# Kernel optimization log

Hardware: AMD Instinct MI355X
Metric: run time of the kernel (lower is better)

Reference implementation:

```python
import jax, jax.numpy as jnp
import numpy as np

H = 128
TYPES = ['user', 'news', 'source', 'follower']
N = {'user': 200000, 'news': 100000, 'source': 5000, 'follower': 200000}
IN = {'user': 128, 'news': 300, 'source': 128, 'follower': 128}
OUT = 2
# relation r: REL_SRC[r] -> REL_DST[r]; order: posts, posted_by, publishes, published_by, follows, followed_by
REL_SRC = ['user', 'news', 'source', 'news', 'follower', 'user']
REL_DST = ['news', 'user', 'news', 'source', 'user', 'follower']
DST_RELS = {'user': [1, 4], 'news': [0, 2], 'source': [3], 'follower': [5]}
E_POSTS, E_PUB, E_FOL = 500000, 100000, 1000000


def _graph_conv(h_src, src, dst, n_src, n_dst, W, b):
    # DGL GraphConv, norm='both': D_dst^{-1/2} A D_src^{-1/2} X W + b (degrees clamped at 1)
    ones = jnp.ones(src.shape[0], h_src.dtype)
    deg_out = jnp.maximum(jax.ops.segment_sum(ones, src, num_segments=n_src), 1.0)
    deg_in = jnp.maximum(jax.ops.segment_sum(ones, dst, num_segments=n_dst), 1.0)
    msg = (h_src * jax.lax.rsqrt(deg_out)[:, None])[src]  # [E, H] gather
    agg = jax.ops.segment_sum(msg, dst, num_segments=n_dst) * jax.lax.rsqrt(deg_in)[:, None]
    return agg @ W + b


def _hetero(ktype, h, edges, Wset, bset):
    # HeteroGraphConv aggregate='mean': mean over relations whose dst type is ktype
    outs = [_graph_conv(h[REL_SRC[r]], edges[r][0], edges[r][1], N[REL_SRC[r]], N[ktype], Wset[r], bset[r])
            for r in DST_RELS[ktype]]
    return sum(outs) / len(outs)


def setup_inputs():
    key = jax.random.key(0)
    ks = iter(jax.random.split(key, 40))
    d = {}
    for t in TYPES:
        d['x_' + t] = jax.random.normal(next(ks), (N[t], IN[t]), jnp.float32)
    for t in TYPES:
        d['Wi1_' + t] = jax.random.normal(next(ks), (IN[t], H), jnp.float32) / np.sqrt(IN[t]).astype(np.float32)
        d['bi1_' + t] = jnp.zeros((H,), jnp.float32)
    d['Wi2'] = jax.random.normal(next(ks), (4, H, H), jnp.float32) / np.float32(np.sqrt(H))
    d['bi2'] = jnp.zeros((4, H), jnp.float32)
    for name in ['conv1', 'conv2']:
        d[name + '_W'] = jax.random.normal(next(ks), (4, 6, H, H), jnp.float32) / np.float32(np.sqrt(H))
        d[name + '_b'] = jnp.zeros((4, 6, H), jnp.float32)
    for t in TYPES:
        d['Wl_' + t] = jax.random.normal(next(ks), (H, OUT), jnp.float32) / np.float32(np.sqrt(H))
        d['bl_' + t] = jnp.zeros((OUT,), jnp.float32)
    d['posts_u'] = jax.random.randint(next(ks), (E_POSTS,), 0, N['user'])
    d['posts_n'] = jax.random.randint(next(ks), (E_POSTS,), 0, N['news'])
    d['pub_s'] = jax.random.randint(next(ks), (E_PUB,), 0, N['source'])
    d['pub_n'] = jax.random.randint(next(ks), (E_PUB,), 0, N['news'])
    d['fol_f'] = jax.random.randint(next(ks), (E_FOL,), 0, N['follower'])
    d['fol_u'] = jax.random.randint(next(ks), (E_FOL,), 0, N['user'])
    return d


def reference(x_user, x_news, x_source, x_follower,
              Wi1_user, bi1_user, Wi1_news, bi1_news, Wi1_source, bi1_source, Wi1_follower, bi1_follower,
              Wi2, bi2, conv1_W, conv1_b, conv2_W, conv2_b,
              Wl_user, bl_user, Wl_news, bl_news, Wl_source, bl_source, Wl_follower, bl_follower,
              posts_u, posts_n, pub_s, pub_n, fol_f, fol_u):
    lrelu = lambda v: jax.nn.leaky_relu(v, 0.01)
    edges = [(posts_u, posts_n), (posts_n, posts_u), (pub_s, pub_n),
             (pub_n, pub_s), (fol_f, fol_u), (fol_u, fol_f)]
    x = {'user': x_user, 'news': x_news, 'source': x_source, 'follower': x_follower}
    Wi1 = {'user': Wi1_user, 'news': Wi1_news, 'source': Wi1_source, 'follower': Wi1_follower}
    bi1 = {'user': bi1_user, 'news': bi1_news, 'source': bi1_source, 'follower': bi1_follower}
    Wl = {'user': Wl_user, 'news': Wl_news, 'source': Wl_source, 'follower': Wl_follower}
    bl = {'user': bl_user, 'news': bl_news, 'source': bl_source, 'follower': bl_follower}
    h = {t: lrelu(x[t] @ Wi1[t] + bi1[t]) for t in TYPES}
    h = {t: lrelu(h[t] @ Wi2[i] + bi2[i]) for i, t in enumerate(TYPES)}
    h = {t: lrelu(_hetero(t, h, edges, conv1_W[i], conv1_b[i])) for i, t in enumerate(TYPES)}
    h1 = {t: lrelu(_hetero(t, h, edges, conv2_W[i], conv2_b[i])) for i, t in enumerate(TYPES)}
    out = {t: h1[t] @ Wl[t] + bl[t] for t in TYPES}
    # original returns ({type: logits}, {type: h1}); flatten to a tuple in TYPES order
    return tuple(out[t] for t in TYPES) + tuple(h1[t] for t in TYPES)
```

## Files before the change

### kernel.cpp

```cpp
#include <hip/hip_runtime.h>

typedef unsigned short u16;
typedef unsigned int   u32;
using short8  = __attribute__((ext_vector_type(8))) short;
using short4v = __attribute__((ext_vector_type(4))) short;
using f32x4   = __attribute__((ext_vector_type(4))) float;
using f32x2   = __attribute__((ext_vector_type(2))) float;

#define N_USER 200000
#define N_NEWS 100000
#define N_SRCT 5000
#define N_FOLW 200000
#define E_POSTS 500000
#define E_PUB   100000
#define E_FOLL  1000000
#define NCNT    805000
#define NPOOL   3200000

__device__ __forceinline__ float bf2f(u16 h) {
  union { u32 u; float f; } v; v.u = ((u32)h) << 16; return v.f;
}
__device__ __forceinline__ u16 f2bf(float f) {
  union { float f; u32 u; } v; v.f = f;
  u32 r = v.u + 0x7FFFu + ((v.u >> 16) & 1u);
  return (u16)(r >> 16);
}

__global__ void count_k(const int* __restrict__ idx, int n, int* __restrict__ cnt) {
  int i = blockIdx.x * 256 + threadIdx.x;
  if (i < n) atomicAdd(&cnt[idx[i]], 1);
}
__global__ void rsqrt_k(const int* __restrict__ cnti, float* __restrict__ out, int n) {
  int i = blockIdx.x * 256 + threadIdx.x;
  if (i < n) {
    int c = cnti[i];
    out[i] = rsqrtf((float)(c > 0 ? c : 1));
  }
}

__global__ void scan1_k(const int* __restrict__ in, int* __restrict__ out,
                        int* __restrict__ bsum, int n) {
  __shared__ int s[256];
  int tid = threadIdx.x;
  int gid = blockIdx.x * 256 + tid;
  int v = (gid < n) ? in[gid] : 0;
  s[tid] = v;
  __syncthreads();
  for (int d = 1; d < 256; d <<= 1) {
    int t = (tid >= d) ? s[tid - d] : 0;
    __syncthreads();
    s[tid] += t;
    __syncthreads();
  }
  if (gid < n) out[gid] = s[tid];
  if (tid == 255) bsum[blockIdx.x] = s[255];
}
__global__ void scan2_k(int* __restrict__ bsum, int m) {
  __shared__ int p[256];
  __shared__ int buf[3328];
  int tid = threadIdx.x;
  int chunk = (m + 255) / 256;
  int run = 0;
  for (int i = 0; i < chunk; ++i) {
    int idx = tid * chunk + i;
    int v = (idx < m) ? bsum[idx] : 0;
    if (idx < m) buf[idx] = run;
    run += v;
  }
  p[tid] = run;
  __syncthreads();
  int own = run;
  for (int d = 1; d < 256; d <<= 1) {
    int t = (tid >= d) ? p[tid - d] : 0;
    __syncthreads();
    p[tid] += t;
    __syncthreads();
  }
  int base = p[tid] - own;
  for (int i = 0; i < chunk; ++i) {
    int idx = tid * chunk + i;
    if (idx < m) bsum[idx] = buf[idx] + base;
  }
}
__global__ void scan3_k(int* __restrict__ offs, const int* __restrict__ cnti,
                        const int* __restrict__ bsum, int n) {
  int gid = blockIdx.x * 256 + threadIdx.x;
  if (gid < n) offs[gid] = offs[gid] - cnti[gid] + bsum[blockIdx.x];
}

__global__ void csr_fill_k(const int* __restrict__ src, const int* __restrict__ dst,
                           const int* __restrict__ offs, int* __restrict__ curs,
                           int* __restrict__ pool, int E, int cntOff) {
  int e = blockIdx.x * 256 + threadIdx.x;
  if (e >= E) return;
  int d = dst[e] + cntOff;
  int p = offs[d] + atomicAdd(&curs[d], 1);
  pool[p] = src[e];
}

__global__ void cvt_pad8_k(const float* __restrict__ X, u16* __restrict__ P,
                           int Ksrc, int Kdst, int total8) {
  int i = blockIdx.x * 256 + threadIdx.x;
  if (i >= total8) return;
  int base = i * 8;
  short8 o;
  if (Ksrc == Kdst) {
    f32x4 a = *(const f32x4*)(X + base);
    f32x4 b = *(const f32x4*)(X + base + 4);
#pragma unroll
    for (int j = 0; j < 4; ++j) { o[j] = (short)f2bf(a[j]); o[j + 4] = (short)f2bf(b[j]); }
  } else {
    int row = base / Kdst;
    int k = base - row * Kdst;
#pragma unroll
    for (int j = 0; j < 8; ++j) {
      int kk = k + j;
      o[j] = (kk < Ksrc) ? (short)f2bf(X[(size_t)row * Ksrc + kk]) : (short)0;
    }
  }
  *(short8*)(P + base) = o;
}

__global__ void trans_w_k(const float* __restrict__ W, u16* __restrict__ WT,
                          int Ksrc, int Kdst, int total) {
  int i = blockIdx.x * 256 + threadIdx.x;
  if (i >= total) return;
  int per = Kdst << 7;
  int m = i / per, rem = i - m * per;
  int n = rem / Kdst, k = rem - n * Kdst;
  WT[i] = (k < Ksrc) ? f2bf(W[(size_t)m * Ksrc * 128 + (size_t)k * 128 + n]) : (u16)0;
}

__global__ __launch_bounds__(256, 2) void gemm_bf16(
    const u16* __restrict__ A, int lda, int M, int K,
    const u16* __restrict__ WT,
    const float* __restrict__ bias,
    const float* __restrict__ rowscale,
    u16* __restrict__ C, int leaky)
{
  __shared__ u16 Ws[128][136];
  const int tid  = threadIdx.x;
  const int wave = tid >> 6;
  const int lane = tid & 63;
  const int l15  = lane & 15;
  const int l4   = lane >> 4;
  const int rowBase = blockIdx.x * 128 + wave * 32;

  f32x4 acc[2][8];
#pragma unroll
  for (int g = 0; g < 2; ++g)
#pragma unroll
    for (int c = 0; c < 8; ++c) acc[g][c] = (f32x4){0.f, 0.f, 0.f, 0.f};

  const int r0 = (rowBase + l15 < M) ? rowBase + l15 : M - 1;
  const int r1 = (rowBase + 16 + l15 < M) ? rowBase + 16 + l15 : M - 1;

  for (int kb = 0; kb < K; kb += 128) {
    const int chunkK = (K - kb < 128) ? (K - kb) : 128;
    __syncthreads();
    for (int fl = tid * 8; fl < (chunkK << 7); fl += 2048) {
      int n = fl / chunkK;
      int kk = fl - n * chunkK;
      *(short8*)(&Ws[n][kk]) = *(const short8*)(WT + (size_t)n * K + kb + kk);
    }
    __syncthreads();
    const int nsteps = chunkK >> 5;
    for (int ks = 0; ks < nsteps; ++ks) {
      const int kg = ks * 32 + l4 * 8;
      short8 a0 = *(const short8*)(A + (size_t)r0 * lda + kb + kg);
      short8 a1 = *(const short8*)(A + (size_t)r1 * lda + kb + kg);
#pragma unroll
      for (int c = 0; c < 8; ++c) {
        short8 b = *(const short8*)(&Ws[c * 16 + l15][kg]);
        acc[0][c] = __builtin_amdgcn_mfma_f32_16x16x32_bf16(a0, b, acc[0][c], 0, 0, 0);
        acc[1][c] = __builtin_amdgcn_mfma_f32_16x16x32_bf16(a1, b, acc[1][c], 0, 0, 0);
      }
    }
  }

  float bvals[8];
#pragma unroll
  for (int c = 0; c < 8; ++c) bvals[c] = bias ? bias[c * 16 + l15] : 0.f;

#pragma unroll
  for (int g = 0; g < 2; ++g) {
#pragma unroll
    for (int r = 0; r < 4; ++r) {
      int row = rowBase + g * 16 + l4 * 4 + r;
      if (row >= M) continue;
      float sc = rowscale ? rowscale[row] : 1.f;
#pragma unroll
      for (int c = 0; c < 8; ++c) {
        float v = acc[g][c][r] * sc + bvals[c];
        if (leaky) v = (v > 0.f) ? v : 0.01f * v;
        C[(size_t)row * 128 + c * 16 + l15] = f2bf(v);
      }
    }
  }
}

__global__ __launch_bounds__(256) void gather_conv(
    const u16* __restrict__ T, const int* __restrict__ pool,
    const int* __restrict__ offs, const int* __restrict__ cnti,
    const float* __restrict__ rsin,
    int co0, int to0, int co1, int to1,
    const float* __restrict__ b1, const float* __restrict__ b2, float invn,
    u16* __restrict__ out_bf, float* __restrict__ out_f, int nDst)
{
  const int wave = threadIdx.x >> 6;
  const int lane = threadIdx.x & 63;
  const int sub  = lane >> 4;
  const int l15  = lane & 15;
  const int d = blockIdx.x * 4 + wave;
  if (d >= nDst) return;

  float s[8];
#pragma unroll
  for (int j = 0; j < 8; ++j) s[j] = 0.f;

  int co = co0, to = to0;
#pragma unroll 1
  for (int r = 0; r < 2; ++r) {
    if (co < 0) break;
    const int off = offs[co + d];
    const int cnt = cnti[co + d];
    const float sc = rsin[co + d];
    float p[8];
#pragma unroll
    for (int j = 0; j < 8; ++j) p[j] = 0.f;
#pragma unroll 1
    for (int e = 0; e < cnt; e += 4) {
      int ee = e + sub;
      bool valid = ee < cnt;
      int idx = pool[off + (valid ? ee : cnt - 1)];
      short8 w = *(const short8*)(T + (((size_t)(to + idx)) << 7) + l15 * 8);
      if (valid) {
#pragma unroll
        for (int j = 0; j < 8; ++j) p[j] += bf2f((u16)w[j]);
      }
    }
#pragma unroll
    for (int j = 0; j < 8; ++j) s[j] += p[j] * sc;
    co = co1; to = to1;
  }

#pragma unroll
  for (int j = 0; j < 8; ++j) {
    s[j] += __shfl_xor(s[j], 16, 64);
    s[j] += __shfl_xor(s[j], 32, 64);
  }

  if (sub == 0) {
    const int col = l15 * 8;
    float v[8];
#pragma unroll
    for (int j = 0; j < 8; ++j) {
      float bb = b1[col + j] + (b2 ? b2[col + j] : 0.f);
      float x = (s[j] + bb) * invn;
      v[j] = (x > 0.f) ? x : 0.01f * x;
    }
    if (out_f) {
      float* op = out_f + (((size_t)d) << 7) + col;
      *(f32x4*)op       = (f32x4){v[0], v[1], v[2], v[3]};
      *(f32x4*)(op + 4) = (f32x4){v[4], v[5], v[6], v[7]};
    } else {
      short8 o;
#pragma unroll
      for (int j = 0; j < 8; ++j) o[j] = (short)f2bf(v[j]);
      *(short8*)(out_bf + (((size_t)d) << 7) + col) = o;
    }
  }
}

__global__ __launch_bounds__(256) void linear_k(
    const float* __restrict__ H, const float* __restrict__ Wl,
    const float* __restrict__ bl, float* __restrict__ OUT, int rows)
{
  __shared__ float w0[128], w1[128];
  int tid = threadIdx.x;
  if (tid < 128) { w0[tid] = Wl[tid * 2]; w1[tid] = Wl[tid * 2 + 1]; }
  __syncthreads();
  int row = blockIdx.x * 256 + tid;
  if (row >= rows) return;
  const float* hp = H + ((size_t)row << 7);
  float s0 = 0.f, s1 = 0.f;
#pragma unroll
  for (int k = 0; k < 128; k += 4) {
    f32x4 h4 = *(const f32x4*)(hp + k);
#pragma unroll
    for (int j = 0; j < 4; ++j) {
      s0 += h4[j] * w0[k + j];
      s1 += h4[j] * w1[k + j];
    }
  }
  OUT[(size_t)row * 2]     = s0 + bl[0];
  OUT[(size_t)row * 2 + 1] = s1 + bl[1];
}

extern "C" void kernel_launch(void* const* d_in, const int* in_sizes, int n_in,
                              void* d_out, int out_size, void* d_ws, size_t ws_size,
                              hipStream_t stream)
{
  (void)in_sizes; (void)n_in; (void)out_size; (void)ws_size;

  char* wp = (char*)d_ws;
  auto take = [&](size_t bytes) { void* p = wp; wp += (bytes + 255) & ~(size_t)255; return p; };
  u16*   ARENA = (u16*)take(206080000);
  u16*   HA  = (u16*)take(129280000);
  u16*   HB  = (u16*)take(129280000);
  u16*   WTA = (u16*)take(1884160);
  float* CNT = (float*)take(3220000);
  int*   CNTI = (int*)take(3220000);
  int*   OFFS = (int*)take(3220000);
  int*   CURS = (int*)take(3220000);
  int*   POOL = (int*)take(12800000);
  int*   BSUM = (int*)take(16384);
  u16*   XB  = ARENA;
  u16*   TP  = ARENA;

  const int rowOff[4] = {0, 200000, 300000, 305000};
  const int Nt[4]     = {N_USER, N_NEWS, N_SRCT, N_FOLW};
  const size_t XOFF[4] = {0, 25600000, 57600000, 58240000};
  const int KD[4] = {128, 320, 128, 128};
  const int KS[4] = {128, 300, 128, 128};
  const int WT1[4] = {0, 16384, 57344, 73728};
  const int WT2 = 90112, WTC1 = 155648, WTC2 = 548864;

  struct RelG { int E, srcIdx, dstIdx, srcType, dstType, srcCnt, dstCnt, tOff; };
  const RelG rels[6] = {
    {E_POSTS, 26, 27, 0, 1, 0,      200000, 0},
    {E_POSTS, 27, 26, 1, 0, 200000, 0,      200000},
    {E_PUB,   28, 29, 2, 1, 300000, 305000, 300000},
    {E_PUB,   29, 28, 1, 2, 305000, 300000, 305000},
    {E_FOLL,  30, 31, 3, 0, 405000, 605000, 405000},
    {E_FOLL,  31, 30, 0, 3, 605000, 405000, 605000},
  };

  hipMemsetAsync(CNTI, 0, NCNT * 4, stream);
  count_k<<<(E_POSTS + 255) / 256, 256, 0, stream>>>((const int*)d_in[26], E_POSTS, CNTI + 0);
  count_k<<<(E_POSTS + 255) / 256, 256, 0, stream>>>((const int*)d_in[27], E_POSTS, CNTI + 200000);
  count_k<<<(E_PUB   + 255) / 256, 256, 0, stream>>>((const int*)d_in[28], E_PUB,   CNTI + 300000);
  count_k<<<(E_PUB   + 255) / 256, 256, 0, stream>>>((const int*)d_in[29], E_PUB,   CNTI + 305000);
  count_k<<<(E_FOLL  + 255) / 256, 256, 0, stream>>>((const int*)d_in[30], E_FOLL,  CNTI + 405000);
  count_k<<<(E_FOLL  + 255) / 256, 256, 0, stream>>>((const int*)d_in[31], E_FOLL,  CNTI + 605000);
  rsqrt_k<<<(NCNT + 255) / 256, 256, 0, stream>>>(CNTI, CNT, NCNT);

  const int scanBlocks = (NCNT + 255) / 256;
  scan1_k<<<scanBlocks, 256, 0, stream>>>(CNTI, OFFS, BSUM, NCNT);
  scan2_k<<<1, 256, 0, stream>>>(BSUM, scanBlocks);
  scan3_k<<<scanBlocks, 256, 0, stream>>>(OFFS, CNTI, BSUM, NCNT);
  hipMemsetAsync(CURS, 0, NCNT * 4, stream);
  for (int r = 0; r < 6; ++r) {
    csr_fill_k<<<(rels[r].E + 255) / 256, 256, 0, stream>>>(
        (const int*)d_in[rels[r].srcIdx], (const int*)d_in[rels[r].dstIdx],
        OFFS, CURS, POOL, rels[r].E, rels[r].dstCnt);
  }

  for (int t = 0; t < 4; ++t) {
    int total8 = (Nt[t] * KD[t]) / 8;
    cvt_pad8_k<<<(total8 + 255) / 256, 256, 0, stream>>>(
        (const float*)d_in[t], XB + XOFF[t], KS[t], KD[t], total8);
  }
  auto transL = [&](int idx, int wtOff, int Ksrc, int Kdst, int total) {
    trans_w_k<<<(total + 255) / 256, 256, 0, stream>>>(
        (const float*)d_in[idx], WTA + wtOff, Ksrc, Kdst, total);
  };
  transL(4,  WT1[0], 128, 128, 16384);
  transL(6,  WT1[1], 300, 320, 40960);
  transL(8,  WT1[2], 128, 128, 16384);
  transL(10, WT1[3], 128, 128, 16384);
  transL(12, WT2,    128, 128, 65536);
  transL(14, WTC1,   128, 128, 393216);
  transL(16, WTC2,   128, 128, 393216);

  auto gemmL = [&](const u16* A, int lda, int M, int K, const u16* WTp,
                   const float* bias, const float* rs, u16* C, int leaky) {
    gemm_bf16<<<(M + 127) / 128, 256, 0, stream>>>(A, lda, M, K, WTp, bias, rs, C, leaky);
  };

  for (int t = 0; t < 4; ++t)
    gemmL(XB + XOFF[t], KD[t], Nt[t], KD[t], WTA + WT1[t],
          (const float*)d_in[5 + 2 * t], nullptr, HA + (size_t)rowOff[t] * 128, 1);

  for (int t = 0; t < 4; ++t)
    gemmL(HA + (size_t)rowOff[t] * 128, 128, Nt[t], 128, WTA + WT2 + t * 16384,
          (const float*)d_in[13] + t * 128, nullptr, HB + (size_t)rowOff[t] * 128, 1);

  const size_t H1OFF[4] = {1010000, 26610000, 39410000, 40050000};
  const size_t LOFF[4]  = {0, 400000, 600000, 610000};
  const int relsOf[4][2] = {{1, 4}, {0, 2}, {3, -1}, {5, -1}};
  float* OUT = (float*)d_out;

  for (int layer = 0; layer < 2; ++layer) {
    const u16* HIn     = layer ? HA : HB;
    const u16* wt      = WTA + (layer ? WTC2 : WTC1);
    const float* convb = (const float*)d_in[layer ? 17 : 15];
    for (int r = 0; r < 6; ++r) {
      const RelG& q = rels[r];
      gemmL(HIn + (size_t)rowOff[q.srcType] * 128, 128, Nt[q.srcType], 128,
            wt + (size_t)(q.dstType * 6 + r) * 16384, nullptr, CNT + q.srcCnt,
            TP + (size_t)q.tOff * 128, 0);
    }
    for (int k = 0; k < 4; ++k) {
      int r1 = relsOf[k][0], r2 = relsOf[k][1];
      int co0 = rels[r1].dstCnt, to0 = rels[r1].tOff;
      int co1 = (r2 >= 0) ? rels[r2].dstCnt : -1;
      int to1 = (r2 >= 0) ? rels[r2].tOff : 0;
      const float* b1 = convb + (size_t)(k * 6 + r1) * 128;
      const float* b2 = (r2 >= 0) ? convb + (size_t)(k * 6 + r2) * 128 : nullptr;
      float invn = (r2 >= 0) ? 0.5f : 1.0f;
      u16* obf  = layer ? nullptr : (HA + (size_t)rowOff[k] * 128);
      float* of = layer ? (OUT + H1OFF[k]) : nullptr;
      gather_conv<<<(Nt[k] + 3) / 4, 256, 0, stream>>>(
          TP, POOL, OFFS, CNTI, CNT, co0, to0, co1, to1, b1, b2, invn, obf, of, Nt[k]);
    }
  }

  for (int k = 0; k < 4; ++k)
    linear_k<<<(Nt[k] + 255) / 256, 256, 0, stream>>>(
        OUT + H1OFF[k], (const float*)d_in[18 + 2 * k], (const float*)d_in[19 + 2 * k],
        OUT + LOFF[k], Nt[k]);
}
```

Measured before the change: 2.280 ms.

## Batch preprocessing launches, fuse fp32 input conversion into GEMM, merge gather loops

Several per-relation and per-type launches (degree counting, CSR fill, weight transposes, final linear heads) are folded into single multi-segment kernels to cut launch overhead. The first-layer GEMM now reads fp32 inputs directly and converts them to bf16 in registers, which removes the separate conversion pass and its intermediate buffer. The gather kernel walks both relations in one flat loop with two edges per lane group per iteration, aiming for more memory parallelism. Relation GEMMs are reordered to run just before their consumer gather, which may improve cache locality. In exchange, the GEMM A-loads become fp32 with conversion work, and the boundary constants are hardcoded.

```diff
diff --git a/kernel.cpp b/kernel.cpp
--- a/kernel.cpp
+++ b/kernel.cpp
@@ -26,9 +26,19 @@
   return (u16)(r >> 16);
 }
 
-__global__ void count_k(const int* __restrict__ idx, int n, int* __restrict__ cnt) {
+__global__ void count6_k(const int* __restrict__ p0, const int* __restrict__ p1,
+                         const int* __restrict__ p2, const int* __restrict__ p3,
+                         const int* __restrict__ p4, const int* __restrict__ p5,
+                         int* __restrict__ cnt) {
   int i = blockIdx.x * 256 + threadIdx.x;
-  if (i < n) atomicAdd(&cnt[idx[i]], 1);
+  const int* p; int off;
+  if      (i < 500000)  { p = p0; off = 0; }
+  else if (i < 1000000) { p = p1; i -= 500000;  off = 200000; }
+  else if (i < 1100000) { p = p2; i -= 1000000; off = 300000; }
+  else if (i < 1200000) { p = p3; i -= 1100000; off = 305000; }
+  else if (i < 2200000) { p = p4; i -= 1200000; off = 405000; }
+  else                  { p = p5; i -= 2200000; off = 605000; }
+  atomicAdd(&cnt[off + p[i]], 1);
 }
 __global__ void rsqrt_k(const int* __restrict__ cnti, float* __restrict__ out, int n) {
   int i = blockIdx.x * 256 + threadIdx.x;
@@ -88,51 +98,71 @@
   if (gid < n) offs[gid] = offs[gid] - cnti[gid] + bsum[blockIdx.x];
 }
 
-__global__ void csr_fill_k(const int* __restrict__ src, const int* __restrict__ dst,
-                           const int* __restrict__ offs, int* __restrict__ curs,
-                           int* __restrict__ pool, int E, int cntOff) {
-  int e = blockIdx.x * 256 + threadIdx.x;
-  if (e >= E) return;
-  int d = dst[e] + cntOff;
-  int p = offs[d] + atomicAdd(&curs[d], 1);
-  pool[p] = src[e];
-}
-
-__global__ void cvt_pad8_k(const float* __restrict__ X, u16* __restrict__ P,
-                           int Ksrc, int Kdst, int total8) {
+__global__ void fill6_k(const int* __restrict__ s0, const int* __restrict__ d0,
+                        const int* __restrict__ s1, const int* __restrict__ d1,
+                        const int* __restrict__ s2, const int* __restrict__ d2,
+                        const int* __restrict__ s3, const int* __restrict__ d3,
+                        const int* __restrict__ s4, const int* __restrict__ d4,
+                        const int* __restrict__ s5, const int* __restrict__ d5,
+                        const int* __restrict__ offs, int* __restrict__ curs,
+                        int* __restrict__ pool) {
   int i = blockIdx.x * 256 + threadIdx.x;
-  if (i >= total8) return;
-  int base = i * 8;
-  short8 o;
-  if (Ksrc == Kdst) {
-    f32x4 a = *(const f32x4*)(X + base);
-    f32x4 b = *(const f32x4*)(X + base + 4);
-#pragma unroll
-    for (int j = 0; j < 4; ++j) { o[j] = (short)f2bf(a[j]); o[j + 4] = (short)f2bf(b[j]); }
-  } else {
-    int row = base / Kdst;
-    int k = base - row * Kdst;
-#pragma unroll
-    for (int j = 0; j < 8; ++j) {
-      int kk = k + j;
-      o[j] = (kk < Ksrc) ? (short)f2bf(X[(size_t)row * Ksrc + kk]) : (short)0;
-    }
-  }
-  *(short8*)(P + base) = o;
-}
-
+  const int* sp; const int* dp; int off;
+  if      (i < 500000)  { sp = s0; dp = d0; off = 200000; }
+  else if (i < 1000000) { sp = s1; dp = d1; i -= 500000;  off = 0; }
+  else if (i < 1100000) { sp = s2; dp = d2; i -= 1000000; off = 305000; }
+  else if (i < 1200000) { sp = s3; dp = d3; i -= 1100000; off = 300000; }
+  else if (i < 2200000) { sp = s4; dp = d4; i -= 1200000; off = 605000; }
+  else                  { sp = s5; dp = d5; i -= 2200000; off = 405000; }
+  int dd = dp[i] + off;
+  int p = offs[dd] + atomicAdd(&curs[dd], 1);
+  pool[p] = sp[i];
+}
+
+__global__ void trans55_k(const float* __restrict__ w0, const float* __restrict__ w1,
+                          const float* __restrict__ w2, const float* __restrict__ w3,
+                          const float* __restrict__ w4, const float* __restrict__ w5,
+                          u16* __restrict__ WT) {
+  int i = blockIdx.x * 256 + threadIdx.x;
+  int m = i >> 14, rem = i & 16383;
+  int n = rem >> 7, k = rem & 127;
+  const float* W; int lm, dstOff;
+  if      (m < 1)  { W = w0; lm = m;      dstOff = 0; }
+  else if (m < 2)  { W = w1; lm = m - 1;  dstOff = 57344; }
+  else if (m < 3)  { W = w2; lm = m - 2;  dstOff = 73728; }
+  else if (m < 7)  { W = w3; lm = m - 3;  dstOff = 90112; }
+  else if (m < 31) { W = w4; lm = m - 7;  dstOff = 155648; }
+  else             { W = w5; lm = m - 31; dstOff = 548864; }
+  WT[dstOff + (lm << 14) + (n << 7) + k] = f2bf(W[(size_t)(lm << 14) + (k << 7) + n]);
+}
 __global__ void trans_w_k(const float* __restrict__ W, u16* __restrict__ WT,
                           int Ksrc, int Kdst, int total) {
   int i = blockIdx.x * 256 + threadIdx.x;
   if (i >= total) return;
-  int per = Kdst << 7;
-  int m = i / per, rem = i - m * per;
-  int n = rem / Kdst, k = rem - n * Kdst;
-  WT[i] = (k < Ksrc) ? f2bf(W[(size_t)m * Ksrc * 128 + (size_t)k * 128 + n]) : (u16)0;
+  int n = i / Kdst, k = i - n * Kdst;
+  WT[i] = (k < Ksrc) ? f2bf(W[(size_t)k * 128 + n]) : (u16)0;
+}
+
+__device__ __forceinline__ short8 ldA32(const float* __restrict__ rowp, int Ks, int k0) {
+  short8 a;
+  if (k0 + 8 <= Ks) {
+    f32x4 u = *(const f32x4*)(rowp + k0);
+    f32x4 v = *(const f32x4*)(rowp + k0 + 4);
+#pragma unroll
+    for (int j = 0; j < 4; ++j) { a[j] = (short)f2bf(u[j]); a[j + 4] = (short)f2bf(v[j]); }
+  } else {
+#pragma unroll
+    for (int j = 0; j < 8; ++j) {
+      int kk = k0 + j;
+      a[j] = (kk < Ks) ? (short)f2bf(rowp[kk]) : (short)0;
+    }
+  }
+  return a;
 }
 
 __global__ __launch_bounds__(256, 2) void gemm_bf16(
-    const u16* __restrict__ A, int lda, int M, int K,
+    const u16* __restrict__ A, const float* __restrict__ A32, int Ks,
+    int lda, int M, int K,
     const u16* __restrict__ WT,
     const float* __restrict__ bias,
     const float* __restrict__ rowscale,
@@ -167,8 +197,14 @@
     const int nsteps = chunkK >> 5;
     for (int ks = 0; ks < nsteps; ++ks) {
       const int kg = ks * 32 + l4 * 8;
-      short8 a0 = *(const short8*)(A + (size_t)r0 * lda + kb + kg);
-      short8 a1 = *(const short8*)(A + (size_t)r1 * lda + kb + kg);
+      short8 a0, a1;
+      if (A32) {
+        a0 = ldA32(A32 + (size_t)r0 * lda, Ks, kb + kg);
+        a1 = ldA32(A32 + (size_t)r1 * lda, Ks, kb + kg);
+      } else {
+        a0 = *(const short8*)(A + (size_t)r0 * lda + kb + kg);
+        a1 = *(const short8*)(A + (size_t)r1 * lda + kb + kg);
+      }
 #pragma unroll
       for (int c = 0; c < 8; ++c) {
         short8 b = *(const short8*)(&Ws[c * 16 + l15][kg]);
@@ -214,34 +250,40 @@
   const int d = blockIdx.x * 4 + wave;
   if (d >= nDst) return;
 
+  const int off0 = offs[co0 + d];
+  const int cnt0 = cnti[co0 + d];
+  const float sc0 = rsin[co0 + d];
+  int off1 = 0, cnt1 = 0; float sc1 = 0.f;
+  if (co1 >= 0) { off1 = offs[co1 + d]; cnt1 = cnti[co1 + d]; sc1 = rsin[co1 + d]; }
+  const int tot = cnt0 + cnt1;
+
   float s[8];
 #pragma unroll
   for (int j = 0; j < 8; ++j) s[j] = 0.f;
 
-  int co = co0, to = to0;
-#pragma unroll 1
-  for (int r = 0; r < 2; ++r) {
-    if (co < 0) break;
-    const int off = offs[co + d];
-    const int cnt = cnti[co + d];
-    const float sc = rsin[co + d];
-    float p[8];
-#pragma unroll
-    for (int j = 0; j < 8; ++j) p[j] = 0.f;
-#pragma unroll 1
-    for (int e = 0; e < cnt; e += 4) {
-      int ee = e + sub;
-      bool valid = ee < cnt;
-      int idx = pool[off + (valid ? ee : cnt - 1)];
-      short8 w = *(const short8*)(T + (((size_t)(to + idx)) << 7) + l15 * 8);
-      if (valid) {
-#pragma unroll
-        for (int j = 0; j < 8; ++j) p[j] += bf2f((u16)w[j]);
-      }
-    }
-#pragma unroll
-    for (int j = 0; j < 8; ++j) s[j] += p[j] * sc;
-    co = co1; to = to1;
+  for (int e = 0; e < tot; e += 8) {
+    const int eA = e + sub;
+    const int eB = e + 4 + sub;
+    if (eA < tot) {
+      bool f0 = eA < cnt0;
+      int pi = f0 ? (off0 + eA) : (off1 + (eA - cnt0));
+      float sc = f0 ? sc0 : sc1;
+      int tb = f0 ? to0 : to1;
+      int idx = pool[pi];
+      short8 w = *(const short8*)(T + (((size_t)(tb + idx)) << 7) + l15 * 8);
+#pragma unroll
+      for (int j = 0; j < 8; ++j) s[j] += bf2f((u16)w[j]) * sc;
+    }
+    if (eB < tot) {
+      bool f0 = eB < cnt0;
+      int pi = f0 ? (off0 + eB) : (off1 + (eB - cnt0));
+      float sc = f0 ? sc0 : sc1;
+      int tb = f0 ? to0 : to1;
+      int idx = pool[pi];
+      short8 w = *(const short8*)(T + (((size_t)(tb + idx)) << 7) + l15 * 8);
+#pragma unroll
+      for (int j = 0; j < 8; ++j) s[j] += bf2f((u16)w[j]) * sc;
+    }
   }
 
 #pragma unroll
@@ -272,29 +314,47 @@
   }
 }
 
-__global__ __launch_bounds__(256) void linear_k(
-    const float* __restrict__ H, const float* __restrict__ Wl,
-    const float* __restrict__ bl, float* __restrict__ OUT, int rows)
+__global__ __launch_bounds__(256) void linear_all_k(
+    const float* __restrict__ Wu, const float* __restrict__ bu,
+    const float* __restrict__ Wn, const float* __restrict__ bn,
+    const float* __restrict__ Wsrc, const float* __restrict__ bsrc,
+    const float* __restrict__ Wf, const float* __restrict__ bfo,
+    float* __restrict__ OUT)
 {
-  __shared__ float w0[128], w1[128];
+  __shared__ float wsh[4][2][128];
+  __shared__ float bsh[4][2];
   int tid = threadIdx.x;
-  if (tid < 128) { w0[tid] = Wl[tid * 2]; w1[tid] = Wl[tid * 2 + 1]; }
+  if (tid < 128) {
+    wsh[0][0][tid] = Wu[tid * 2];   wsh[0][1][tid] = Wu[tid * 2 + 1];
+    wsh[1][0][tid] = Wn[tid * 2];   wsh[1][1][tid] = Wn[tid * 2 + 1];
+    wsh[2][0][tid] = Wsrc[tid * 2]; wsh[2][1][tid] = Wsrc[tid * 2 + 1];
+    wsh[3][0][tid] = Wf[tid * 2];   wsh[3][1][tid] = Wf[tid * 2 + 1];
+  } else if (tid < 132) {
+    int t = tid - 128;
+    const float* bp = (t == 0) ? bu : (t == 1) ? bn : (t == 2) ? bsrc : bfo;
+    bsh[t][0] = bp[0]; bsh[t][1] = bp[1];
+  }
   __syncthreads();
   int row = blockIdx.x * 256 + tid;
-  if (row >= rows) return;
-  const float* hp = H + ((size_t)row << 7);
+  if (row >= 505000) return;
+  int t, lr; size_t hoff; int loff;
+  if      (row < 200000) { t = 0; lr = row;          hoff = 1010000;  loff = 0; }
+  else if (row < 300000) { t = 1; lr = row - 200000; hoff = 26610000; loff = 400000; }
+  else if (row < 305000) { t = 2; lr = row - 300000; hoff = 39410000; loff = 600000; }
+  else                   { t = 3; lr = row - 305000; hoff = 40050000; loff = 610000; }
+  const float* hp = OUT + hoff + (size_t)lr * 128;
   float s0 = 0.f, s1 = 0.f;
 #pragma unroll
   for (int k = 0; k < 128; k += 4) {
     f32x4 h4 = *(const f32x4*)(hp + k);
 #pragma unroll
     for (int j = 0; j < 4; ++j) {
-      s0 += h4[j] * w0[k + j];
-      s1 += h4[j] * w1[k + j];
-    }
-  }
-  OUT[(size_t)row * 2]     = s0 + bl[0];
-  OUT[(size_t)row * 2 + 1] = s1 + bl[1];
+      s0 += h4[j] * wsh[t][0][k + j];
+      s1 += h4[j] * wsh[t][1][k + j];
+    }
+  }
+  OUT[(size_t)loff + lr * 2]     = s0 + bsh[t][0];
+  OUT[(size_t)loff + lr * 2 + 1] = s1 + bsh[t][1];
 }
 
 extern "C" void kernel_launch(void* const* d_in, const int* in_sizes, int n_in,
@@ -305,7 +365,7 @@
 
   char* wp = (char*)d_ws;
   auto take = [&](size_t bytes) { void* p = wp; wp += (bytes + 255) & ~(size_t)255; return p; };
-  u16*   ARENA = (u16*)take(206080000);
+  u16*   TP  = (u16*)take(206080000);
   u16*   HA  = (u16*)take(129280000);
   u16*   HB  = (u16*)take(129280000);
   u16*   WTA = (u16*)take(1884160);
@@ -315,12 +375,9 @@
   int*   CURS = (int*)take(3220000);
   int*   POOL = (int*)take(12800000);
   int*   BSUM = (int*)take(16384);
-  u16*   XB  = ARENA;
-  u16*   TP  = ARENA;
 
   const int rowOff[4] = {0, 200000, 300000, 305000};
   const int Nt[4]     = {N_USER, N_NEWS, N_SRCT, N_FOLW};
-  const size_t XOFF[4] = {0, 25600000, 57600000, 58240000};
   const int KD[4] = {128, 320, 128, 128};
   const int KS[4] = {128, 300, 128, 128};
   const int WT1[4] = {0, 16384, 57344, 73728};
@@ -337,12 +394,9 @@
   };
 
   hipMemsetAsync(CNTI, 0, NCNT * 4, stream);
-  count_k<<<(E_POSTS + 255) / 256, 256, 0, stream>>>((const int*)d_in[26], E_POSTS, CNTI + 0);
-  count_k<<<(E_POSTS + 255) / 256, 256, 0, stream>>>((const int*)d_in[27], E_POSTS, CNTI + 200000);
-  count_k<<<(E_PUB   + 255) / 256, 256, 0, stream>>>((const int*)d_in[28], E_PUB,   CNTI + 300000);
-  count_k<<<(E_PUB   + 255) / 256, 256, 0, stream>>>((const int*)d_in[29], E_PUB,   CNTI + 305000);
-  count_k<<<(E_FOLL  + 255) / 256, 256, 0, stream>>>((const int*)d_in[30], E_FOLL,  CNTI + 405000);
-  count_k<<<(E_FOLL  + 255) / 256, 256, 0, stream>>>((const int*)d_in[31], E_FOLL,  CNTI + 605000);
+  count6_k<<<12500, 256, 0, stream>>>(
+      (const int*)d_in[26], (const int*)d_in[27], (const int*)d_in[28],
+      (const int*)d_in[29], (const int*)d_in[30], (const int*)d_in[31], CNTI);
   rsqrt_k<<<(NCNT + 255) / 256, 256, 0, stream>>>(CNTI, CNT, NCNT);
 
   const int scanBlocks = (NCNT + 255) / 256;
@@ -350,44 +404,35 @@
   scan2_k<<<1, 256, 0, stream>>>(BSUM, scanBlocks);
   scan3_k<<<scanBlocks, 256, 0, stream>>>(OFFS, CNTI, BSUM, NCNT);
   hipMemsetAsync(CURS, 0, NCNT * 4, stream);
-  for (int r = 0; r < 6; ++r) {
-    csr_fill_k<<<(rels[r].E + 255) / 256, 256, 0, stream>>>(
-        (const int*)d_in[rels[r].srcIdx], (const int*)d_in[rels[r].dstIdx],
-        OFFS, CURS, POOL, rels[r].E, rels[r].dstCnt);
-  }
-
-  for (int t = 0; t < 4; ++t) {
-    int total8 = (Nt[t] * KD[t]) / 8;
-    cvt_pad8_k<<<(total8 + 255) / 256, 256, 0, stream>>>(
-        (const float*)d_in[t], XB + XOFF[t], KS[t], KD[t], total8);
-  }
-  auto transL = [&](int idx, int wtOff, int Ksrc, int Kdst, int total) {
-    trans_w_k<<<(total + 255) / 256, 256, 0, stream>>>(
-        (const float*)d_in[idx], WTA + wtOff, Ksrc, Kdst, total);
+  fill6_k<<<12500, 256, 0, stream>>>(
+      (const int*)d_in[26], (const int*)d_in[27],
+      (const int*)d_in[27], (const int*)d_in[26],
+      (const int*)d_in[28], (const int*)d_in[29],
+      (const int*)d_in[29], (const int*)d_in[28],
+      (const int*)d_in[30], (const int*)d_in[31],
+      (const int*)d_in[31], (const int*)d_in[30],
+      OFFS, CURS, POOL);
+
+  trans55_k<<<3520, 256, 0, stream>>>(
+      (const float*)d_in[4], (const float*)d_in[8], (const float*)d_in[10],
+      (const float*)d_in[12], (const float*)d_in[14], (const float*)d_in[16], WTA);
+  trans_w_k<<<(40960 + 255) / 256, 256, 0, stream>>>(
+      (const float*)d_in[6], WTA + WT1[1], 300, 320, 40960);
+
+  auto gemmL = [&](const u16* A, const float* A32, int Ks, int lda, int M, int K,
+                   const u16* WTp, const float* bias, const float* rs, u16* C, int leaky) {
+    gemm_bf16<<<(M + 127) / 128, 256, 0, stream>>>(A, A32, Ks, lda, M, K, WTp, bias, rs, C, leaky);
   };
-  transL(4,  WT1[0], 128, 128, 16384);
-  transL(6,  WT1[1], 300, 320, 40960);
-  transL(8,  WT1[2], 128, 128, 16384);
-  transL(10, WT1[3], 128, 128, 16384);
-  transL(12, WT2,    128, 128, 65536);
-  transL(14, WTC1,   128, 128, 393216);
-  transL(16, WTC2,   128, 128, 393216);
-
-  auto gemmL = [&](const u16* A, int lda, int M, int K, const u16* WTp,
-                   const float* bias, const float* rs, u16* C, int leaky) {
-    gemm_bf16<<<(M + 127) / 128, 256, 0, stream>>>(A, lda, M, K, WTp, bias, rs, C, leaky);
-  };
 
   for (int t = 0; t < 4; ++t)
-    gemmL(XB + XOFF[t], KD[t], Nt[t], KD[t], WTA + WT1[t],
+    gemmL(nullptr, (const float*)d_in[t], KS[t], KS[t], Nt[t], KD[t], WTA + WT1[t],
           (const float*)d_in[5 + 2 * t], nullptr, HA + (size_t)rowOff[t] * 128, 1);
 
   for (int t = 0; t < 4; ++t)
-    gemmL(HA + (size_t)rowOff[t] * 128, 128, Nt[t], 128, WTA + WT2 + t * 16384,
+    gemmL(HA + (size_t)rowOff[t] * 128, nullptr, 0, 128, Nt[t], 128, WTA + WT2 + t * 16384,
           (const float*)d_in[13] + t * 128, nullptr, HB + (size_t)rowOff[t] * 128, 1);
 
   const size_t H1OFF[4] = {1010000, 26610000, 39410000, 40050000};
-  const size_t LOFF[4]  = {0, 400000, 600000, 610000};
   const int relsOf[4][2] = {{1, 4}, {0, 2}, {3, -1}, {5, -1}};
   float* OUT = (float*)d_out;
 
@@ -395,14 +440,16 @@
     const u16* HIn     = layer ? HA : HB;
     const u16* wt      = WTA + (layer ? WTC2 : WTC1);
     const float* convb = (const float*)d_in[layer ? 17 : 15];
-    for (int r = 0; r < 6; ++r) {
-      const RelG& q = rels[r];
-      gemmL(HIn + (size_t)rowOff[q.srcType] * 128, 128, Nt[q.srcType], 128,
-            wt + (size_t)(q.dstType * 6 + r) * 16384, nullptr, CNT + q.srcCnt,
-            TP + (size_t)q.tOff * 128, 0);
-    }
     for (int k = 0; k < 4; ++k) {
       int r1 = relsOf[k][0], r2 = relsOf[k][1];
+      for (int j = 0; j < 2; ++j) {
+        int r = relsOf[k][j];
+        if (r < 0) continue;
+        const RelG& q = rels[r];
+        gemmL(HIn + (size_t)rowOff[q.srcType] * 128, nullptr, 0, 128, Nt[q.srcType], 128,
+              wt + (size_t)(q.dstType * 6 + r) * 16384, nullptr, CNT + q.srcCnt,
+              TP + (size_t)q.tOff * 128, 0);
+      }
       int co0 = rels[r1].dstCnt, to0 = rels[r1].tOff;
       int co1 = (r2 >= 0) ? rels[r2].dstCnt : -1;
       int to1 = (r2 >= 0) ? rels[r2].tOff : 0;
@@ -416,8 +463,9 @@
     }
   }
 
-  for (int k = 0; k < 4; ++k)
-    linear_k<<<(Nt[k] + 255) / 256, 256, 0, stream>>>(
-        OUT + H1OFF[k], (const float*)d_in[18 + 2 * k], (const float*)d_in[19 + 2 * k],
-        OUT + LOFF[k], Nt[k]);
-}
+  linear_all_k<<<(505000 + 255) / 256, 256, 0, stream>>>(
+      (const float*)d_in[18], (const float*)d_in[19],
+      (const float*)d_in[20], (const float*)d_in[21],
+      (const float*)d_in[22], (const float*)d_in[23],
+      (const float*)d_in[24], (const float*)d_in[25], OUT);
+}
```

New measurement: 2.024 ms. -11.2%, faster.
